# Optimization experiments

Hardware: AMD Instinct MI355X
Metric: run time of the kernel (lower is better)

The kernel has to match this reference:

```python
import jax, jax.numpy as jnp
import numpy as np
from jax import lax

B, S, C, V, D, NC, NF, H = 8, 1024, 512, 512, 512, 512, 2, 8
TAU = 1.0


def conv1d(x, w, b, stride=1, pad=0):
    # x [B,C,S], w [O,I,K]
    y = lax.conv_general_dilated(x, w, (stride,), [(pad, pad)],
                                 dimension_numbers=('NCW', 'OIW', 'NCW'))
    return y + b[None, :, None]


def conv_transpose1d(x, w, b):
    # torch ConvTranspose1d(k=2, s=2); w [I,O,K]
    y = lax.conv_transpose(x, w, (2,), 'VALID',
                           dimension_numbers=('NCW', 'IOW', 'NCW'),
                           transpose_kernel=True)
    return y + b[None, :, None]


def resblock(x, ws, bs):
    h = x
    for i in range(3):
        h = conv1d(jax.nn.elu(h), ws[i], bs[i])
    return h + x


def layernorm(x, g, b):
    m = x.mean(-1, keepdims=True)
    v = ((x - m) ** 2).mean(-1, keepdims=True)
    return (x - m) / jnp.sqrt(v + 1e-5) * g + b


def mha(x, in_w, in_b, out_w, out_b):
    # x [S,B,C], torch nn.MultiheadAttention (eval, no dropout)
    S_, B_, C_ = x.shape
    hd = C_ // H
    qkv = x @ in_w.T + in_b            # [S,B,3C]
    q, k, v = jnp.split(qkv, 3, axis=-1)
    q = q.reshape(S_, B_, H, hd)
    k = k.reshape(S_, B_, H, hd)
    v = v.reshape(S_, B_, H, hd)
    att = jnp.einsum('sbhd,tbhd->bhst', q, k) / np.sqrt(hd).astype(np.float32)
    att = jax.nn.softmax(att, axis=-1)
    o = jnp.einsum('bhst,tbhd->sbhd', att, v).reshape(S_, B_, C_)
    return o @ out_w.T + out_b


def setup_inputs() -> dict:
    key = jax.random.key(0)
    ks = iter(jax.random.split(key, 64))
    def w(shape, s=0.02):
        return jax.random.normal(next(ks), shape, jnp.float32) * s
    inp = {}
    inp['x'] = jax.random.randint(next(ks), (B, S), 0, V, jnp.int32)
    inp['embed'] = w((V, C)).at[0].set(0.0)  # padding_idx=0
    inp['enc_res_w'] = w((3, C, C, 1)); inp['enc_res_b'] = w((3, C))
    inp['enc_in_w'] = w((3 * C, C)); inp['enc_in_b'] = w((3 * C,))
    inp['enc_out_w'] = w((C, C)); inp['enc_out_b'] = w((C,))
    inp['enc_ln_g'] = jnp.ones((C,), jnp.float32); inp['enc_ln_b'] = jnp.zeros((C,), jnp.float32)
    inp['enc_down_w'] = w((NF, C, C, 2)); inp['enc_down_b'] = w((NF, C))
    inp['e2q_w'] = w((D, C, 3)); inp['e2q_b'] = w((D,))
    inp['codebook'] = jax.random.normal(next(ks), (D, NC), jnp.float32)  # [dim, n_embed]
    inp['q2d_w'] = w((C, D, 3)); inp['q2d_b'] = w((C,))
    inp['dec_res_w'] = w((NF, 3, C, C, 1)); inp['dec_res_b'] = w((NF, 3, C))
    inp['dec_in_w'] = w((NF, 3 * C, C)); inp['dec_in_b'] = w((NF, 3 * C))
    inp['dec_out_w'] = w((NF, C, C)); inp['dec_out_b'] = w((NF, C))
    inp['dec_ln_g'] = jnp.ones((NF, C), jnp.float32); inp['dec_ln_b'] = jnp.zeros((NF, C), jnp.float32)
    inp['dec_up_w'] = w((NF, C, C, 2)); inp['dec_up_b'] = w((NF, C))
    return inp


def reference(x, embed, enc_res_w, enc_res_b, enc_in_w, enc_in_b, enc_out_w,
              enc_out_b, enc_ln_g, enc_ln_b, enc_down_w, enc_down_b, e2q_w,
              e2q_b, codebook, q2d_w, q2d_b, dec_res_w, dec_res_b, dec_in_w,
              dec_in_b, dec_out_w, dec_out_b, dec_ln_g, dec_ln_b, dec_up_w,
              dec_up_b):
    # ---- encode ----
    h = embed[x]                       # [B,S,C]
    h = h.transpose(0, 2, 1)           # [B,C,S]
    h = resblock(h, enc_res_w, enc_res_b)
    t = h.transpose(2, 0, 1)           # [S,B,C]
    t = layernorm(mha(t, enc_in_w, enc_in_b, enc_out_w, enc_out_b) + t,
                  enc_ln_g, enc_ln_b)
    h = t.transpose(1, 2, 0)           # [B,C,S]
    for i in range(NF):
        h = conv1d(h, enc_down_w[i], enc_down_b[i], stride=2)
    h = conv1d(h, e2q_w, e2q_b, pad=1)  # [B,D,S4]
    z_e = h.transpose(0, 2, 1)          # [B,S4,D]
    # ---- VQ quantize (eval) ----
    flat = z_e.reshape(-1, D)
    dist = ((flat ** 2).sum(1, keepdims=True)
            - 2.0 * flat @ codebook
            + (codebook ** 2).sum(0)[None, :])
    ids = jnp.argmin(dist, axis=1).reshape(z_e.shape[0], -1)  # [B,S4]
    q = codebook.T[ids]                 # [B,S4,D]
    diff = jnp.mean((lax.stop_gradient(q) - z_e) ** 2)
    z = z_e + lax.stop_gradient(q - z_e)  # straight-through
    # ---- decode ----
    h = z.transpose(0, 2, 1)            # [B,D,S4]
    h = conv1d(h, q2d_w, q2d_b, pad=1)  # [B,C,S4]
    for i in range(NF):
        h = resblock(h, dec_res_w[i], dec_res_b[i])
        t = h.transpose(2, 0, 1)
        t = layernorm(mha(t, dec_in_w[i], dec_in_b[i], dec_out_w[i], dec_out_b[i]) + t,
                      dec_ln_g[i], dec_ln_b[i])
        h = t.transpose(1, 2, 0)
        h = conv_transpose1d(h, dec_up_w[i], dec_up_b[i])
    h = h.transpose(0, 2, 1)            # [B,S,C]
    logp = jax.nn.log_softmax(h / TAU, axis=-1)
    return logp, z, diff, ids
```

## Files before the change

### kernel.cpp

```cpp
#include <hip/hip_runtime.h>
#include <hip/hip_bf16.h>


static constexpr size_t SLOT = 4194304;

typedef short bf16x8 __attribute__((ext_vector_type(8)));
typedef float f32x4  __attribute__((ext_vector_type(4)));

__device__ __forceinline__ float eluf(float x) { return x > 0.f ? x : expm1f(x); }
__device__ __forceinline__ short f2bf(float v) {
  unsigned u = __float_as_uint(v);
  return (short)((u + 0x7FFFu + ((u >> 16) & 1u)) >> 16);
}
__device__ __forceinline__ float bf2f(short s) {
  return __uint_as_float(((unsigned)(unsigned short)s) << 16);
}

__global__ __launch_bounds__(256) void gemm_k(
    const float* __restrict__ A, const float* __restrict__ W,
    const float* __restrict__ bias, const float* __restrict__ res,
    float* __restrict__ Y, int P, int K, int O,
    int act, int accum, int smod, int shift, int ystride, int yoff,
    int WS, int nseg)
{
  __shared__ alignas(16) float As[16][68];
  __shared__ alignas(16) float Bs[16][68];
  const int tid = threadIdx.x;
  const int bp = blockIdx.x * 64, bo = blockIdx.y * 64;
  const int tx = tid & 15, ty = tid >> 4;
  const int srow = tid >> 2, skq = (tid & 3) << 2;
  float vout[4][4];

  for (int seg = 0; seg < nseg; seg++) {
    const int sh = (nseg == 3) ? (seg - 1) : shift;
    const float* Wseg = (nseg == 3) ? (W + (size_t)seg * 262144) : W;
    float acc[4][4];
#pragma unroll
    for (int i = 0; i < 4; i++)
#pragma unroll
      for (int j = 0; j < 4; j++) acc[i][j] = 0.f;

    bool aok = true;
    if (smod) { const int s = (bp + srow) & (smod - 1); aok = ((unsigned)(s + sh) < (unsigned)smod); }
    const float* arow = A + (size_t)(bp + srow + sh) * K;
    const float* brow = Wseg + (size_t)(bo + srow) * WS;

    float4 pa = aok ? *(const float4*)&arow[skq] : make_float4(0.f, 0.f, 0.f, 0.f);
    float4 pb = *(const float4*)&brow[skq];

    for (int k0 = 0; k0 < K; k0 += 16) {
      if (act) { pa.x = eluf(pa.x); pa.y = eluf(pa.y); pa.z = eluf(pa.z); pa.w = eluf(pa.w); }
      __syncthreads();
      As[skq + 0][srow] = pa.x; As[skq + 1][srow] = pa.y;
      As[skq + 2][srow] = pa.z; As[skq + 3][srow] = pa.w;
      Bs[skq + 0][srow] = pb.x; Bs[skq + 1][srow] = pb.y;
      Bs[skq + 2][srow] = pb.z; Bs[skq + 3][srow] = pb.w;
      __syncthreads();
      const int kn = (k0 + 16 < K) ? (k0 + 16 + skq) : (k0 + skq);
      pa = aok ? *(const float4*)&arow[kn] : make_float4(0.f, 0.f, 0.f, 0.f);
      pb = *(const float4*)&brow[kn];
#pragma unroll
      for (int kk2 = 0; kk2 < 16; kk2++) {
        const float4 av = *(const float4*)&As[kk2][ty * 4];
        const float4 bv = *(const float4*)&Bs[kk2][tx * 4];
        const float a_[4] = {av.x, av.y, av.z, av.w};
        const float b_[4] = {bv.x, bv.y, bv.z, bv.w};
#pragma unroll
        for (int i = 0; i < 4; i++)
#pragma unroll
          for (int j = 0; j < 4; j++) acc[i][j] += a_[i] * b_[j];
      }
    }
    if (seg == 0) {
#pragma unroll
      for (int i = 0; i < 4; i++)
#pragma unroll
        for (int j = 0; j < 4; j++) {
          float t = acc[i][j];
          if (nseg == 3 && bias) t += bias[bo + tx * 4 + j];
          vout[i][j] = t;
        }
    } else {
#pragma unroll
      for (int i = 0; i < 4; i++)
#pragma unroll
        for (int j = 0; j < 4; j++) vout[i][j] = acc[i][j] + vout[i][j];
    }
  }
#pragma unroll
  for (int i = 0; i < 4; i++) {
    const int p = bp + ty * 4 + i;
    const size_t yrow = (size_t)p * ystride + yoff;
#pragma unroll
    for (int j = 0; j < 4; j++) {
      const int o = bo + tx * 4 + j;
      float v = vout[i][j];
      if (nseg == 1) {
        if (bias) v += bias[o];
        if (res)  v += res[(size_t)p * O + o];
        if (accum) v += Y[yrow * O + o];
      }
      Y[yrow * O + o] = v;
    }
  }
}

static inline void launch_gemm(hipStream_t st, const float* A, const float* W,
                               const float* bias, const float* res, float* Y,
                               int P, int K, int O, int act, int accum,
                               int smod, int shift, int ystride, int yoff,
                               int WS, int nseg)
{
  dim3 g(P / 64, O / 64);
  gemm_k<<<g, 256, 0, st>>>(A, W, bias, res, Y, P, K, O, act, accum, smod, shift,
                            ystride, yoff, WS, nseg);
}

__global__ __launch_bounds__(256) void bgemm_k(
    const short* __restrict__ A, const short* __restrict__ W,
    const float* __restrict__ bias, const float* __restrict__ res,
    float* __restrict__ Y, int P, int O, int accum,
    int smod, int shift, int ystride, int yoff,
    short* __restrict__ Yb, int bact, int k3)
{
  __shared__ short As[4096];
  __shared__ short Bs[4096];
  const int tid = threadIdx.x;
  const int lane = tid & 63, wid = tid >> 6;
  const int wr = wid >> 1, wc = wid & 1;
  const int bp = blockIdx.x * 64, bo = blockIdx.y * 64;
  f32x4 acc[2][2];
#pragma unroll
  for (int mi = 0; mi < 2; mi++)
#pragma unroll
    for (int ni = 0; ni < 2; ni++) acc[mi][ni] = (f32x4){0.f, 0.f, 0.f, 0.f};

  const int nseg = k3 ? 3 : 1;
  for (int seg = 0; seg < nseg; seg++) {
    const int sh = k3 ? (seg - 1) : shift;
    const int sm = k3 ? 256 : smod;
    const short* Wseg = W + (size_t)seg * 262144;
    for (int k0 = 0; k0 < 512; k0 += 64) {
#pragma unroll
      for (int c0 = 0; c0 < 2; c0++) {
        const int c = tid + c0 * 256;
        const int row = c >> 3, kc = c & 7;
        int soff = (row << 6) + (kc << 3); soff ^= (row & 7) << 3;
        const int p = bp + row;
        bf16x8 av = {0, 0, 0, 0, 0, 0, 0, 0};
        bool ok = true;
        if (sm) { const int s = p & (sm - 1); ok = ((unsigned)(s + sh) < (unsigned)sm); }
        if (ok) av = *(const bf16x8*)&A[(size_t)(p + sh) * 512 + k0 + (kc << 3)];
        *(bf16x8*)&As[soff] = av;
        *(bf16x8*)&Bs[soff] = *(const bf16x8*)&Wseg[(size_t)(bo + row) * 512 + k0 + (kc << 3)];
      }
      __syncthreads();
#pragma unroll
      for (int ks = 0; ks < 2; ks++) {
        bf16x8 af[2], bfr[2];
#pragma unroll
        for (int mi = 0; mi < 2; mi++) {
          const int row = wr * 32 + mi * 16 + (lane & 15);
          int soff = (row << 6) + (ks << 5) + ((lane >> 4) << 3);
          soff ^= (row & 7) << 3;
          af[mi] = *(const bf16x8*)&As[soff];
        }
#pragma unroll
        for (int ni = 0; ni < 2; ni++) {
          const int row = wc * 32 + ni * 16 + (lane & 15);
          int soff = (row << 6) + (ks << 5) + ((lane >> 4) << 3);
          soff ^= (row & 7) << 3;
          bfr[ni] = *(const bf16x8*)&Bs[soff];
        }
#pragma unroll
        for (int mi = 0; mi < 2; mi++)
#pragma unroll
          for (int ni = 0; ni < 2; ni++)
            acc[mi][ni] = __builtin_amdgcn_mfma_f32_16x16x32_bf16(af[mi], bfr[ni], acc[mi][ni], 0, 0, 0);
      }
      __syncthreads();
    }
  }
#pragma unroll
  for (int mi = 0; mi < 2; mi++)
#pragma unroll
    for (int ni = 0; ni < 2; ni++)
#pragma unroll
      for (int r = 0; r < 4; r++) {
        const int p = bp + wr * 32 + mi * 16 + ((lane >> 4) << 2) + r;
        const int o = bo + wc * 32 + ni * 16 + (lane & 15);
        float v = acc[mi][ni][r];
        if (bias) v += bias[o];
        if (res)  v += res[(size_t)p * O + o];
        const size_t yi = ((size_t)p * ystride + yoff) * O + o;
        if (accum) v += Y[yi];
        if (Y) Y[yi] = v;
        if (Yb) Yb[yi] = f2bf(bact ? eluf(v) : v);
      }
}

__global__ __launch_bounds__(512) void battn_k(
    const short* __restrict__ qkv, float* __restrict__ Oa,
    short* __restrict__ Ob, int S)
{
  __shared__ short sq[8192];
  __shared__ short sk[4096];
  __shared__ short svt[4096];
  const int tid = threadIdx.x;
  const int lane = tid & 63, w = tid >> 6;
  const int bl = blockIdx.y >> 3, h = blockIdx.y & 7;
  const int q0 = blockIdx.x * 128;
  const short* base = qkv + (size_t)bl * S * 1536 + h * 64;

  {
    const int row = tid >> 2, c0 = (tid & 3) << 4;
    const short* src = base + (size_t)(q0 + row) * 1536 + c0;
    bf16x8 v0 = *(const bf16x8*)&src[0];
    bf16x8 v1 = *(const bf16x8*)&src[8];
#pragma unroll
    for (int e = 0; e < 8; e++) {
      v0[e] = f2bf(bf2f(v0[e]) * 0.125f);
      v1[e] = f2bf(bf2f(v1[e]) * 0.125f);
    }
    int s0 = (row << 6) + c0;       s0 ^= (row & 7) << 3;
    int s1 = (row << 6) + c0 + 8;   s1 ^= (row & 7) << 3;
    *(bf16x8*)&sq[s0] = v0; *(bf16x8*)&sq[s1] = v1;
  }
  __syncthreads();
  bf16x8 af[2];
#pragma unroll
  for (int ks = 0; ks < 2; ks++) {
    const int row = (w << 4) + (lane & 15);
    int soff = (row << 6) + (((lane >> 4) + 4 * ks) << 3);
    soff ^= (row & 7) << 3;
    af[ks] = *(const bf16x8*)&sq[soff];
  }

  f32x4 oacc[4];
#pragma unroll
  for (int dt = 0; dt < 4; dt++) oacc[dt] = (f32x4){0.f, 0.f, 0.f, 0.f};
  float m[4], l[4];
#pragma unroll
  for (int r = 0; r < 4; r++) { m[r] = -INFINITY; l[r] = 0.f; }

  for (int t0 = 0; t0 < S; t0 += 64) {
    __syncthreads();
    if (tid < 256) {
      const int row = tid >> 2, c0 = (tid & 3) << 4;
      const short* ksrc = base + (size_t)(t0 + row) * 1536 + 512 + c0;
      int s0 = (row << 6) + c0;       s0 ^= (row & 7) << 3;
      int s1 = (row << 6) + c0 + 8;   s1 ^= (row & 7) << 3;
      *(bf16x8*)&sk[s0] = *(const bf16x8*)&ksrc[0];
      *(bf16x8*)&sk[s1] = *(const bf16x8*)&ksrc[8];
    } else {
      const int t = tid - 256;
      const int row = t >> 2, c0 = (t & 3) << 4;
      const short* vsrc = base + (size_t)(t0 + row) * 1536 + 1024 + c0;
      const bf16x8 va0 = *(const bf16x8*)&vsrc[0];
      const bf16x8 va1 = *(const bf16x8*)&vsrc[8];
#pragma unroll
      for (int i = 0; i < 16; i++) {
        const int dd = c0 + i;
        int so = (dd << 6) + row;
        so ^= ((dd & 7) ^ (((dd >> 4) & 3) << 1)) << 3;
        svt[so] = (i < 8) ? va0[i & 7] : va1[i & 7];
      }
    }
    __syncthreads();
    f32x4 sacc[4];
#pragma unroll
    for (int ct = 0; ct < 4; ct++) {
      sacc[ct] = (f32x4){0.f, 0.f, 0.f, 0.f};
#pragma unroll
      for (int ks = 0; ks < 2; ks++) {
        const int row = (ct << 4) + (lane & 15);
        int soff = (row << 6) + (((lane >> 4) + 4 * ks) << 3);
        soff ^= (row & 7) << 3;
        const bf16x8 bk = *(const bf16x8*)&sk[soff];
        sacc[ct] = __builtin_amdgcn_mfma_f32_16x16x32_bf16(af[ks], bk, sacc[ct], 0, 0, 0);
      }
    }
    float p[4][4]; float corr[4];
#pragma unroll
    for (int r = 0; r < 4; r++) {
      float mx = fmaxf(fmaxf(sacc[0][r], sacc[1][r]), fmaxf(sacc[2][r], sacc[3][r]));
      mx = fmaxf(mx, __shfl_xor(mx, 1));
      mx = fmaxf(mx, __shfl_xor(mx, 2));
      mx = fmaxf(mx, __shfl_xor(mx, 4));
      mx = fmaxf(mx, __shfl_xor(mx, 8));
      const float newm = fmaxf(m[r], mx);
      corr[r] = expf(m[r] - newm);
      float psum = 0.f;
#pragma unroll
      for (int ct = 0; ct < 4; ct++) { p[ct][r] = expf(sacc[ct][r] - newm); psum += p[ct][r]; }
      psum += __shfl_xor(psum, 1);
      psum += __shfl_xor(psum, 2);
      psum += __shfl_xor(psum, 4);
      psum += __shfl_xor(psum, 8);
      l[r] = l[r] * corr[r] + psum;
      m[r] = newm;
#pragma unroll
      for (int dt = 0; dt < 4; dt++) oacc[dt][r] *= corr[r];
    }
#pragma unroll
    for (int r = 0; r < 4; r++)
#pragma unroll
      for (int ct = 0; ct < 4; ct++) {
        const int q = (w << 4) + ((lane >> 4) << 2) + r;
        const int kv = (ct << 4) + (lane & 15);
        int so = (q << 6) + kv; so ^= (q & 7) << 3;
        sq[so] = f2bf(p[ct][r]);
      }
#pragma unroll
    for (int ks = 0; ks < 2; ks++) {
      const int prow = (w << 4) + (lane & 15);
      int poff = (prow << 6) + (((lane >> 4) + 4 * ks) << 3);
      poff ^= (prow & 7) << 3;
      const bf16x8 pa = *(const bf16x8*)&sq[poff];
#pragma unroll
      for (int dt = 0; dt < 4; dt++) {
        const int vrow = (dt << 4) + (lane & 15);
        int voff = (vrow << 6) + (((lane >> 4) + 4 * ks) << 3);
        voff ^= ((vrow & 7) ^ (((vrow >> 4) & 3) << 1)) << 3;
        const bf16x8 bv = *(const bf16x8*)&svt[voff];
        oacc[dt] = __builtin_amdgcn_mfma_f32_16x16x32_bf16(pa, bv, oacc[dt], 0, 0, 0);
      }
    }
  }
#pragma unroll
  for (int r = 0; r < 4; r++) {
    const float inv = 1.f / l[r];
    const int q = (w << 4) + ((lane >> 4) << 2) + r;
    const size_t rowbase = (size_t)(bl * S + q0 + q) * 512 + h * 64;
#pragma unroll
    for (int dt = 0; dt < 4; dt++) {
      const int d = (dt << 4) + (lane & 15);
      const float ov = oacc[dt][r] * inv;
      if (Oa) Oa[rowbase + d] = ov;
      if (Ob) Ob[rowbase + d] = f2bf(ov);
    }
  }
}

__global__ __launch_bounds__(256) void cast_k(const float* __restrict__ src,
    short* __restrict__ dst, int act)
{
  const size_t i = ((size_t)blockIdx.x * 256 + threadIdx.x) * 8;
  float4 a = *(const float4*)&src[i];
  float4 b = *(const float4*)&src[i + 4];
  if (act) {
    a.x = eluf(a.x); a.y = eluf(a.y); a.z = eluf(a.z); a.w = eluf(a.w);
    b.x = eluf(b.x); b.y = eluf(b.y); b.z = eluf(b.z); b.w = eluf(b.w);
  }
  bf16x8 o;
  o[0] = f2bf(a.x); o[1] = f2bf(a.y); o[2] = f2bf(a.z); o[3] = f2bf(a.w);
  o[4] = f2bf(b.x); o[5] = f2bf(b.y); o[6] = f2bf(b.z); o[7] = f2bf(b.w);
  *(bf16x8*)&dst[i] = o;
}

__global__ __launch_bounds__(256) void q2dw_k(const float* __restrict__ src, short* __restrict__ dst)
{
  const int idx = blockIdx.x * 256 + threadIdx.x;
  const int w = idx >> 18, rem = idx & 262143;
  const int o = rem >> 9, k = rem & 511;
  dst[idx] = f2bf(src[(size_t)o * 1536 + k * 3 + w]);
}

__global__ __launch_bounds__(256) void upw_k(const float* __restrict__ src, short* __restrict__ dst)
{
  const int idx = blockIdx.x * 256 + threadIdx.x;
  const int mi = idx >> 18, f = mi >> 1, kq = mi & 1;
  const int rem = idx & 262143;
  const int o = rem >> 9, i2 = rem & 511;
  dst[idx] = f2bf(src[(size_t)f * 524288 + (size_t)i2 * 1024 + o * 2 + kq]);
}

__global__ __launch_bounds__(256) void downw_k(const float* __restrict__ src, float* __restrict__ dst)
{
  const int idx = blockIdx.x * 256 + threadIdx.x;
  const int i = idx & 511, ks = (idx >> 9) & 1, o = idx >> 10;
  dst[idx] = src[(size_t)o * 1024 + i * 2 + ks];
}

__global__ __launch_bounds__(256) void e2qw_k(const float* __restrict__ src, float* __restrict__ dst)
{
  const int idx = blockIdx.x * 256 + threadIdx.x;
  const int w = idx >> 18, rem = idx & 262143;
  const int o = rem >> 9, k = rem & 511;
  dst[idx] = src[(size_t)o * 1536 + k * 3 + w];
}

__global__ __launch_bounds__(256) void cbt_k(const float* __restrict__ src, float* __restrict__ dst)
{
  const int idx = blockIdx.x * 256 + threadIdx.x;
  const int n = idx >> 9, d = idx & 511;
  dst[idx] = src[(size_t)d * 512 + n];
}

__global__ __launch_bounds__(256) void ln_k(const float* __restrict__ X,
    const float* __restrict__ g, const float* __restrict__ bta,
    float* __restrict__ Y, short* __restrict__ Ob)
{
  const int row = blockIdx.x * 4 + (threadIdx.x >> 6);
  const int lane = threadIdx.x & 63;
  const float* x = X + (size_t)row * 512;
  float v[8]; float s = 0.f;
#pragma unroll
  for (int i = 0; i < 8; i++) { v[i] = x[lane + i * 64]; s += v[i]; }
#pragma unroll
  for (int off = 1; off < 64; off <<= 1) s += __shfl_xor(s, off);
  const float mean = s * (1.f / 512.f);
  float vs = 0.f;
#pragma unroll
  for (int i = 0; i < 8; i++) { const float d = v[i] - mean; vs += d * d; }
#pragma unroll
  for (int off = 1; off < 64; off <<= 1) vs += __shfl_xor(vs, off);
  const float rstd = 1.f / sqrtf(vs * (1.f / 512.f) + 1e-5f);
  float* y = Y ? (Y + (size_t)row * 512) : nullptr;
#pragma unroll
  for (int i = 0; i < 8; i++) {
    const int c = lane + i * 64;
    const float o = (v[i] - mean) * rstd * g[c] + bta[c];
    if (y) y[c] = o;
    if (Ob) Ob[(size_t)row * 512 + c] = f2bf(o);
  }
}

__global__ __launch_bounds__(256) void lsm_k(const float* __restrict__ X,
    float* __restrict__ out)
{
  const int row = blockIdx.x * 4 + (threadIdx.x >> 6);
  const int lane = threadIdx.x & 63;
  const float* x = X + (size_t)row * 512;
  float v[8]; float mx = -3.0e38f;
#pragma unroll
  for (int i = 0; i < 8; i++) { v[i] = x[lane + i * 64]; mx = fmaxf(mx, v[i]); }
#pragma unroll
  for (int off = 1; off < 64; off <<= 1) mx = fmaxf(mx, __shfl_xor(mx, off));
  float sum = 0.f;
#pragma unroll
  for (int i = 0; i < 8; i++) sum += expf(v[i] - mx);
#pragma unroll
  for (int off = 1; off < 64; off <<= 1) sum += __shfl_xor(sum, off);
  const float ls = logf(sum);
  float* y = out + (size_t)row * 512;
#pragma unroll
  for (int i = 0; i < 8; i++) y[lane + i * 64] = v[i] - mx - ls;
}

__global__ __launch_bounds__(256) void embed_k(const int* __restrict__ x,
    const float* __restrict__ emb, float* __restrict__ out, short* __restrict__ outb)
{
  const int i = blockIdx.x * 256 + threadIdx.x;
  const int p = i >> 7, c4 = i & 127;
  const int id = x[p];
  const float4 v = *(const float4*)&emb[(size_t)id * 512 + c4 * 4];
  *(float4*)&out[(size_t)p * 512 + c4 * 4] = v;
  short* ob = outb + (size_t)p * 512 + c4 * 4;
  ob[0] = f2bf(eluf(v.x)); ob[1] = f2bf(eluf(v.y));
  ob[2] = f2bf(eluf(v.z)); ob[3] = f2bf(eluf(v.w));
}

__global__ __launch_bounds__(64) void cnorm_k(const float* __restrict__ cbT, float* __restrict__ cn)
{
  const int n = blockIdx.x; const int lane = threadIdx.x;
  float s = 0.f;
#pragma unroll
  for (int i = 0; i < 8; i++) {
    const float v = cbT[(size_t)n * 512 + lane + i * 64];
    s += v * v;
  }
#pragma unroll
  for (int off = 1; off < 64; off <<= 1) s += __shfl_xor(s, off);
  if (lane == 0) cn[n] = s;
}

__global__ __launch_bounds__(256) void argmin_k(const float* __restrict__ scores,
    const float* __restrict__ cn, int* __restrict__ ids,
    float* __restrict__ out_ids)
{
  const int row = blockIdx.x * 4 + (threadIdx.x >> 6);
  const int lane = threadIdx.x & 63;
  const float* sr = scores + (size_t)row * 512;
  float best = 3.0e38f; int bi = 0x7fffffff;
#pragma unroll
  for (int i = 0; i < 8; i++) {
    const int n = lane + i * 64;
    const float v = cn[n] - 2.f * sr[n];
    if (v < best || (v == best && n < bi)) { best = v; bi = n; }
  }
#pragma unroll
  for (int off = 1; off < 64; off <<= 1) {
    const float ov = __shfl_xor(best, off);
    const int oi = __shfl_xor(bi, off);
    if (ov < best || (ov == best && oi < bi)) { best = ov; bi = oi; }
  }
  if (lane == 0) { ids[row] = bi; out_ids[row] = (float)bi; }
}

__global__ __launch_bounds__(128) void zq_k(const float* __restrict__ z_e,
    const float* __restrict__ cbT, const int* __restrict__ ids,
    float* __restrict__ zout, short* __restrict__ zb, float* __restrict__ dpart)
{
  __shared__ float red[2];
  const int p = blockIdx.x, t = threadIdx.x;
  const int id = ids[p];
  const float4 ze = *(const float4*)&z_e[(size_t)p * 512 + t * 4];
  const float4 q4 = *(const float4*)&cbT[(size_t)id * 512 + t * 4];
  const float4 dv = make_float4(q4.x - ze.x, q4.y - ze.y, q4.z - ze.z, q4.w - ze.w);
  const float4 z  = make_float4(ze.x + dv.x, ze.y + dv.y, ze.z + dv.z, ze.w + dv.w);
  *(float4*)&zout[(size_t)p * 512 + t * 4] = z;
  short* zo = zb + (size_t)p * 512 + t * 4;
  zo[0] = f2bf(z.x); zo[1] = f2bf(z.y); zo[2] = f2bf(z.z); zo[3] = f2bf(z.w);
  float loc = dv.x * dv.x + dv.y * dv.y + dv.z * dv.z + dv.w * dv.w;
#pragma unroll
  for (int off = 1; off < 64; off <<= 1) loc += __shfl_xor(loc, off);
  const int lane = t & 63, w = t >> 6;
  if (lane == 0) red[w] = loc;
  __syncthreads();
  if (t == 0) dpart[p] = red[0] + red[1];
}

__global__ __launch_bounds__(256) void diffred_k(const float* __restrict__ dpart,
    float* __restrict__ out_diff)
{
  __shared__ float red[4];
  const int t = threadIdx.x;
  float s = 0.f;
#pragma unroll
  for (int i = 0; i < 8; i++) s += dpart[t + i * 256];
#pragma unroll
  for (int off = 1; off < 64; off <<= 1) s += __shfl_xor(s, off);
  if ((t & 63) == 0) red[t >> 6] = s;
  __syncthreads();
  if (t == 0) out_diff[0] = (red[0] + red[1] + red[2] + red[3]) * (1.f / 1048576.f);
}

extern "C" void kernel_launch(void* const* d_in, const int* in_sizes, int n_in,
                              void* d_out, int out_size, void* d_ws, size_t ws_size,
                              hipStream_t stream)
{
  const int*   x         = (const int*)d_in[0];
  const float* embed     = (const float*)d_in[1];
  const float* enc_res_w = (const float*)d_in[2];
  const float* enc_res_b = (const float*)d_in[3];
  const float* enc_in_w  = (const float*)d_in[4];
  const float* enc_in_b  = (const float*)d_in[5];
  const float* enc_out_w = (const float*)d_in[6];
  const float* enc_out_b = (const float*)d_in[7];
  const float* enc_ln_g  = (const float*)d_in[8];
  const float* enc_ln_b  = (const float*)d_in[9];
  const float* enc_down_w= (const float*)d_in[10];
  const float* enc_down_b= (const float*)d_in[11];
  const float* e2q_w     = (const float*)d_in[12];
  const float* e2q_b     = (const float*)d_in[13];
  const float* codebook  = (const float*)d_in[14];
  const float* q2d_w     = (const float*)d_in[15];
  const float* q2d_b     = (const float*)d_in[16];
  const float* dec_res_w = (const float*)d_in[17];
  const float* dec_res_b = (const float*)d_in[18];
  const float* dec_in_w  = (const float*)d_in[19];
  const float* dec_in_b  = (const float*)d_in[20];
  const float* dec_out_w = (const float*)d_in[21];
  const float* dec_out_b = (const float*)d_in[22];
  const float* dec_ln_g  = (const float*)d_in[23];
  const float* dec_ln_b  = (const float*)d_in[24];
  const float* dec_up_w  = (const float*)d_in[25];
  const float* dec_up_b  = (const float*)d_in[26];

  float* ws = (float*)d_ws;
  float* S0   = ws;
  float* S1   = ws + SLOT;
  float* S2   = ws + 2 * SLOT;
  float* QKVb = ws + 3 * SLOT;
  float* cnorm = QKVb + (size_t)8192 * 1536;
  int*   idsI  = (int*)(cnorm + 512);
  float* dpart = (float*)(idsI + 2048);

  float* out      = (float*)d_out;
  float* out_logp = out;
  float* out_z    = out + 4194304;
  float* out_diff = out + 5242880;
  float* out_ids  = out + 5242881;

  short* q2dWb   = (short*)out_logp;
  short* resWb   = q2dWb + 786432;
  short* inWb    = resWb + 1572864;
  short* outWb   = inWb + 1572864;
  short* upWb    = outWb + 524288;
  short* AbA     = upWb + 1048576;
  short* encResWb= AbA + 2097152;
  short* AbB   = (short*)(QKVb + 8388608);
  short* encInWb  = (short*)out_z;
  short* encOutWb = encInWb + 786432;
  float* dsW      = out_z + 524288;
  short* QKVsh = (short*)QKVb;
  float* e2qT  = QKVb;
  float* ds2W  = QKVb + 786432;
  float* cbT   = QKVb + 1310720;
  short* E0    = (short*)QKVb;
  short* E1    = E0 + 4194304;
  short* S2sh  = (short*)S2;

  q2dw_k<<<3072, 256, 0, stream>>>(q2d_w, q2dWb);
  cast_k<<<768, 256, 0, stream>>>(dec_res_w, resWb, 0);
  cast_k<<<768, 256, 0, stream>>>(dec_in_w,  inWb, 0);
  cast_k<<<256, 256, 0, stream>>>(dec_out_w, outWb, 0);
  upw_k<<<4096, 256, 0, stream>>>(dec_up_w, upWb);
  cast_k<<<384, 256, 0, stream>>>(enc_res_w, encResWb, 0);
  cast_k<<<384, 256, 0, stream>>>(enc_in_w,  encInWb, 0);
  cast_k<<<128, 256, 0, stream>>>(enc_out_w, encOutWb, 0);
  downw_k<<<2048, 256, 0, stream>>>(enc_down_w, dsW);

  embed_k<<<4096, 256, 0, stream>>>(x, embed, S0, E0);
  { dim3 g(128, 8);
    bgemm_k<<<g, 256, 0, stream>>>(E0, encResWb,          enc_res_b,        nullptr, nullptr, 8192, 512, 0, 0, 0, 1, 0, E1, 1, 0);
    bgemm_k<<<g, 256, 0, stream>>>(E1, encResWb + 262144, enc_res_b + 512,  nullptr, nullptr, 8192, 512, 0, 0, 0, 1, 0, E0, 1, 0);
    bgemm_k<<<g, 256, 0, stream>>>(E0, encResWb + 524288, enc_res_b + 1024, S0,      S1, 8192, 512, 0, 0, 0, 1, 0, S2sh, 0, 0);
  }
  { dim3 g(128, 24);
    bgemm_k<<<g, 256, 0, stream>>>(S2sh, encInWb, enc_in_b, nullptr, nullptr, 8192, 1536, 0, 0, 0, 1, 0, QKVsh, 0, 0);
  }
  battn_k<<<dim3(8, 64), 512, 0, stream>>>(QKVsh, nullptr, S2sh, 1024);
  { dim3 g(128, 8);
    bgemm_k<<<g, 256, 0, stream>>>(S2sh, encOutWb, enc_out_b, S1, S0, 8192, 512, 0, 0, 0, 1, 0, nullptr, 0, 0);
  }
  e2qw_k<<<3072, 256, 0, stream>>>(e2q_w, e2qT);
  downw_k<<<2048, 256, 0, stream>>>(enc_down_w + 524288, ds2W);
  cbt_k<<<1024, 256, 0, stream>>>(codebook, cbT);
  cnorm_k<<<512, 64, 0, stream>>>(cbT, cnorm);
  ln_k<<<2048, 256, 0, stream>>>(S0, enc_ln_g, enc_ln_b, S1, nullptr);
  launch_gemm(stream, S1, dsW, enc_down_b, nullptr, S2, 4096, 1024, 512, 0, 0, 0, 0, 1, 0, 1024, 1);
  launch_gemm(stream, S2, ds2W, enc_down_b + 512, nullptr, S0, 2048, 1024, 512, 0, 0, 0, 0, 1, 0, 1024, 1);
  launch_gemm(stream, S0, e2qT, e2q_b, nullptr, S2, 2048, 512, 512, 0, 0, 256, 0, 1, 0, 512, 3);
  launch_gemm(stream, S2, cbT, nullptr, nullptr, S1, 2048, 512, 512, 0, 0, 0, 0, 1, 0, 512, 1);
  argmin_k<<<512, 256, 0, stream>>>(S1, cnorm, idsI, out_ids);
  zq_k<<<2048, 128, 0, stream>>>(S2, cbT, idsI, out_z, AbA, dpart);
  diffred_k<<<1, 256, 0, stream>>>(dpart, out_diff);

  { dim3 g(32, 8);
    bgemm_k<<<g, 256, 0, stream>>>(AbA, q2dWb, q2d_b, nullptr, S1, 2048, 512, 0, 256, 0, 1, 0, AbB, 1, 1);
  }
  { dim3 g(32, 8); dim3 gq(32, 24);
    bgemm_k<<<g, 256, 0, stream>>>(AbB, resWb,            dec_res_b,        nullptr, S2, 2048, 512, 0, 0, 0, 1, 0, AbA, 1, 0);
    bgemm_k<<<g, 256, 0, stream>>>(AbA, resWb + 262144,   dec_res_b + 512,  nullptr, S0, 2048, 512, 0, 0, 0, 1, 0, AbB, 1, 0);
    bgemm_k<<<g, 256, 0, stream>>>(AbB, resWb + 524288,   dec_res_b + 1024, S1,      S2, 2048, 512, 0, 0, 0, 1, 0, AbA, 0, 0);
    bgemm_k<<<gq, 256, 0, stream>>>(AbA, inWb,            dec_in_b,         nullptr, nullptr, 2048, 1536, 0, 0, 0, 1, 0, QKVsh, 0, 0);
    battn_k<<<dim3(2, 64), 512, 0, stream>>>(QKVsh, nullptr, AbB, 256);
    bgemm_k<<<g, 256, 0, stream>>>(AbB, outWb,            dec_out_b,        S2, S1, 2048, 512, 0, 0, 0, 1, 0, nullptr, 0, 0);
    ln_k<<<512, 256, 0, stream>>>(S1, dec_ln_g, dec_ln_b, S2, AbA);
    bgemm_k<<<g, 256, 0, stream>>>(AbA, upWb,             dec_up_b, nullptr, S0, 2048, 512, 0, 0, 0, 2, 0, AbB, 1, 0);
    bgemm_k<<<g, 256, 0, stream>>>(AbA, upWb + 262144,    dec_up_b, nullptr, S0, 2048, 512, 0, 0, 0, 2, 1, AbB, 1, 0);
  }
  { dim3 g(64, 8); dim3 gq(64, 24);
    bgemm_k<<<g, 256, 0, stream>>>(AbB, resWb + 786432,   dec_res_b + 1536, nullptr, S1, 4096, 512, 0, 0, 0, 1, 0, AbA, 1, 0);
    bgemm_k<<<g, 256, 0, stream>>>(AbA, resWb + 1048576,  dec_res_b + 2048, nullptr, S2, 4096, 512, 0, 0, 0, 1, 0, AbB, 1, 0);
    bgemm_k<<<g, 256, 0, stream>>>(AbB, resWb + 1310720,  dec_res_b + 2560, S0,      S1, 4096, 512, 0, 0, 0, 1, 0, AbA, 0, 0);
    bgemm_k<<<gq, 256, 0, stream>>>(AbA, inWb + 786432,   dec_in_b + 1536,  nullptr, nullptr, 4096, 1536, 0, 0, 0, 1, 0, QKVsh, 0, 0);
    battn_k<<<dim3(4, 64), 512, 0, stream>>>(QKVsh, nullptr, AbB, 512);
    bgemm_k<<<g, 256, 0, stream>>>(AbB, outWb + 262144,   dec_out_b + 512,  S1, S0, 4096, 512, 0, 0, 0, 1, 0, nullptr, 0, 0);
    ln_k<<<1024, 256, 0, stream>>>(S0, dec_ln_g + 512, dec_ln_b + 512, S1, AbA);
    bgemm_k<<<g, 256, 0, stream>>>(AbA, upWb + 524288,    dec_up_b + 512, nullptr, S0, 4096, 512, 0, 0, 0, 2, 0, nullptr, 0, 0);
    bgemm_k<<<g, 256, 0, stream>>>(AbA, upWb + 786432,    dec_up_b + 512, nullptr, S0, 4096, 512, 0, 0, 0, 2, 1, nullptr, 0, 0);
  }
  lsm_k<<<2048, 256, 0, stream>>>(S0, out_logp);
}
```

Baseline: 792.9 us.

## Double-buffer shared memory and register-prefetch tiles in both GEMM kernels

```diff
diff --git a/kernel.cpp b/kernel.cpp
--- a/kernel.cpp
+++ b/kernel.cpp
@@ -23,68 +23,83 @@
     int act, int accum, int smod, int shift, int ystride, int yoff,
     int WS, int nseg)
 {
-  __shared__ alignas(16) float As[16][68];
-  __shared__ alignas(16) float Bs[16][68];
+  __shared__ alignas(16) float As[2][16][68];
+  __shared__ alignas(16) float Bs[2][16][68];
   const int tid = threadIdx.x;
   const int bp = blockIdx.x * 64, bo = blockIdx.y * 64;
   const int tx = tid & 15, ty = tid >> 4;
   const int srow = tid >> 2, skq = (tid & 3) << 2;
-  float vout[4][4];
-
-  for (int seg = 0; seg < nseg; seg++) {
-    const int sh = (nseg == 3) ? (seg - 1) : shift;
-    const float* Wseg = (nseg == 3) ? (W + (size_t)seg * 262144) : W;
-    float acc[4][4];
-#pragma unroll
-    for (int i = 0; i < 4; i++)
-#pragma unroll
-      for (int j = 0; j < 4; j++) acc[i][j] = 0.f;
-
-    bool aok = true;
-    if (smod) { const int s = (bp + srow) & (smod - 1); aok = ((unsigned)(s + sh) < (unsigned)smod); }
-    const float* arow = A + (size_t)(bp + srow + sh) * K;
-    const float* brow = Wseg + (size_t)(bo + srow) * WS;
-
-    float4 pa = aok ? *(const float4*)&arow[skq] : make_float4(0.f, 0.f, 0.f, 0.f);
-    float4 pb = *(const float4*)&brow[skq];
-
-    for (int k0 = 0; k0 < K; k0 += 16) {
-      if (act) { pa.x = eluf(pa.x); pa.y = eluf(pa.y); pa.z = eluf(pa.z); pa.w = eluf(pa.w); }
-      __syncthreads();
-      As[skq + 0][srow] = pa.x; As[skq + 1][srow] = pa.y;
-      As[skq + 2][srow] = pa.z; As[skq + 3][srow] = pa.w;
-      Bs[skq + 0][srow] = pb.x; Bs[skq + 1][srow] = pb.y;
-      Bs[skq + 2][srow] = pb.z; Bs[skq + 3][srow] = pb.w;
-      __syncthreads();
-      const int kn = (k0 + 16 < K) ? (k0 + 16 + skq) : (k0 + skq);
-      pa = aok ? *(const float4*)&arow[kn] : make_float4(0.f, 0.f, 0.f, 0.f);
-      pb = *(const float4*)&brow[kn];
-#pragma unroll
-      for (int kk2 = 0; kk2 < 16; kk2++) {
-        const float4 av = *(const float4*)&As[kk2][ty * 4];
-        const float4 bv = *(const float4*)&Bs[kk2][tx * 4];
-        const float a_[4] = {av.x, av.y, av.z, av.w};
-        const float b_[4] = {bv.x, bv.y, bv.z, bv.w};
+  float vout[4][4], acc[4][4];
+#pragma unroll
+  for (int i = 0; i < 4; i++)
+#pragma unroll
+    for (int j = 0; j < 4; j++) acc[i][j] = 0.f;
+
+  const float* arow = nullptr; const float* brow = nullptr; bool aok = true;
+  auto seg_setup = [&](int s) {
+    const int sh = (nseg == 3) ? (s - 1) : shift;
+    const float* Wseg = (nseg == 3) ? (W + (size_t)s * 262144) : W;
+    aok = true;
+    if (smod) { const int ss = (bp + srow) & (smod - 1); aok = ((unsigned)(ss + sh) < (unsigned)smod); }
+    arow = A + (size_t)(bp + srow + sh) * K;
+    brow = Wseg + (size_t)(bo + srow) * WS;
+  };
+  seg_setup(0);
+  float4 pa = aok ? *(const float4*)&arow[skq] : make_float4(0.f, 0.f, 0.f, 0.f);
+  float4 pb = *(const float4*)&brow[skq];
+
+  const int ips = K >> 4;
+  const int niter = nseg * ips;
+  int lkk = 0, lseg = 0, cur = 0, ckk = 0, cseg = 0;
+
+  for (int it = 0; it < niter; ++it) {
+    if (act) { pa.x = eluf(pa.x); pa.y = eluf(pa.y); pa.z = eluf(pa.z); pa.w = eluf(pa.w); }
+    As[cur][skq + 0][srow] = pa.x; As[cur][skq + 1][srow] = pa.y;
+    As[cur][skq + 2][srow] = pa.z; As[cur][skq + 3][srow] = pa.w;
+    Bs[cur][skq + 0][srow] = pb.x; Bs[cur][skq + 1][srow] = pb.y;
+    Bs[cur][skq + 2][srow] = pb.z; Bs[cur][skq + 3][srow] = pb.w;
+    __syncthreads();
+    if (it + 1 < niter) {
+      lkk += 16;
+      if (lkk == K) { lkk = 0; seg_setup(++lseg); }
+      pa = aok ? *(const float4*)&arow[lkk + skq] : make_float4(0.f, 0.f, 0.f, 0.f);
+      pb = *(const float4*)&brow[lkk + skq];
+    }
+#pragma unroll
+    for (int kk2 = 0; kk2 < 16; kk2++) {
+      const float4 av = *(const float4*)&As[cur][kk2][ty * 4];
+      const float4 bv = *(const float4*)&Bs[cur][kk2][tx * 4];
+      const float a_[4] = {av.x, av.y, av.z, av.w};
+      const float b_[4] = {bv.x, bv.y, bv.z, bv.w};
+#pragma unroll
+      for (int i = 0; i < 4; i++)
+#pragma unroll
+        for (int j = 0; j < 4; j++) acc[i][j] += a_[i] * b_[j];
+    }
+    cur ^= 1;
+    ckk += 16;
+    if (ckk == K) {
+      ckk = 0;
+      if (cseg == 0) {
 #pragma unroll
         for (int i = 0; i < 4; i++)
 #pragma unroll
-          for (int j = 0; j < 4; j++) acc[i][j] += a_[i] * b_[j];
-      }
-    }
-    if (seg == 0) {
+          for (int j = 0; j < 4; j++) {
+            float t = acc[i][j];
+            if (nseg == 3 && bias) t += bias[bo + tx * 4 + j];
+            vout[i][j] = t;
+          }
+      } else {
+#pragma unroll
+        for (int i = 0; i < 4; i++)
+#pragma unroll
+          for (int j = 0; j < 4; j++) vout[i][j] = acc[i][j] + vout[i][j];
+      }
 #pragma unroll
       for (int i = 0; i < 4; i++)
 #pragma unroll
-        for (int j = 0; j < 4; j++) {
-          float t = acc[i][j];
-          if (nseg == 3 && bias) t += bias[bo + tx * 4 + j];
-          vout[i][j] = t;
-        }
-    } else {
-#pragma unroll
-      for (int i = 0; i < 4; i++)
-#pragma unroll
-        for (int j = 0; j < 4; j++) vout[i][j] = acc[i][j] + vout[i][j];
+        for (int j = 0; j < 4; j++) acc[i][j] = 0.f;
+      cseg++;
     }
   }
 #pragma unroll
@@ -123,8 +138,8 @@
     int smod, int shift, int ystride, int yoff,
     short* __restrict__ Yb, int bact, int k3)
 {
-  __shared__ short As[4096];
-  __shared__ short Bs[4096];
+  __shared__ short As[2][4096];
+  __shared__ short Bs[2][4096];
   const int tid = threadIdx.x;
   const int lane = tid & 63, wid = tid >> 6;
   const int wr = wid >> 1, wc = wid & 1;
@@ -136,50 +151,68 @@
     for (int ni = 0; ni < 2; ni++) acc[mi][ni] = (f32x4){0.f, 0.f, 0.f, 0.f};
 
   const int nseg = k3 ? 3 : 1;
-  for (int seg = 0; seg < nseg; seg++) {
+  const int niter = nseg * 8;
+  bf16x8 rA[2], rB[2];
+
+  auto stage_load = [&](int it) {
+    const int seg = it >> 3, k0 = (it & 7) << 6;
     const int sh = k3 ? (seg - 1) : shift;
     const int sm = k3 ? 256 : smod;
     const short* Wseg = W + (size_t)seg * 262144;
-    for (int k0 = 0; k0 < 512; k0 += 64) {
-#pragma unroll
-      for (int c0 = 0; c0 < 2; c0++) {
-        const int c = tid + c0 * 256;
-        const int row = c >> 3, kc = c & 7;
-        int soff = (row << 6) + (kc << 3); soff ^= (row & 7) << 3;
-        const int p = bp + row;
-        bf16x8 av = {0, 0, 0, 0, 0, 0, 0, 0};
-        bool ok = true;
-        if (sm) { const int s = p & (sm - 1); ok = ((unsigned)(s + sh) < (unsigned)sm); }
-        if (ok) av = *(const bf16x8*)&A[(size_t)(p + sh) * 512 + k0 + (kc << 3)];
-        *(bf16x8*)&As[soff] = av;
-        *(bf16x8*)&Bs[soff] = *(const bf16x8*)&Wseg[(size_t)(bo + row) * 512 + k0 + (kc << 3)];
-      }
-      __syncthreads();
-#pragma unroll
-      for (int ks = 0; ks < 2; ks++) {
-        bf16x8 af[2], bfr[2];
-#pragma unroll
-        for (int mi = 0; mi < 2; mi++) {
-          const int row = wr * 32 + mi * 16 + (lane & 15);
-          int soff = (row << 6) + (ks << 5) + ((lane >> 4) << 3);
-          soff ^= (row & 7) << 3;
-          af[mi] = *(const bf16x8*)&As[soff];
-        }
-#pragma unroll
-        for (int ni = 0; ni < 2; ni++) {
-          const int row = wc * 32 + ni * 16 + (lane & 15);
-          int soff = (row << 6) + (ks << 5) + ((lane >> 4) << 3);
-          soff ^= (row & 7) << 3;
-          bfr[ni] = *(const bf16x8*)&Bs[soff];
-        }
-#pragma unroll
-        for (int mi = 0; mi < 2; mi++)
-#pragma unroll
-          for (int ni = 0; ni < 2; ni++)
-            acc[mi][ni] = __builtin_amdgcn_mfma_f32_16x16x32_bf16(af[mi], bfr[ni], acc[mi][ni], 0, 0, 0);
-      }
-      __syncthreads();
-    }
+#pragma unroll
+    for (int c0 = 0; c0 < 2; c0++) {
+      const int c = tid + c0 * 256;
+      const int row = c >> 3, kc = c & 7;
+      const int p = bp + row;
+      bf16x8 av = {0, 0, 0, 0, 0, 0, 0, 0};
+      bool ok = true;
+      if (sm) { const int s = p & (sm - 1); ok = ((unsigned)(s + sh) < (unsigned)sm); }
+      if (ok) av = *(const bf16x8*)&A[(size_t)(p + sh) * 512 + k0 + (kc << 3)];
+      rA[c0] = av;
+      rB[c0] = *(const bf16x8*)&Wseg[(size_t)(bo + row) * 512 + k0 + (kc << 3)];
+    }
+  };
+  auto stage_write = [&](int cb) {
+#pragma unroll
+    for (int c0 = 0; c0 < 2; c0++) {
+      const int c = tid + c0 * 256;
+      const int row = c >> 3, kc = c & 7;
+      int soff = (row << 6) + (kc << 3); soff ^= (row & 7) << 3;
+      *(bf16x8*)&As[cb][soff] = rA[c0];
+      *(bf16x8*)&Bs[cb][soff] = rB[c0];
+    }
+  };
+
+  stage_load(0);
+  int cur = 0;
+  for (int it = 0; it < niter; ++it) {
+    stage_write(cur);
+    __syncthreads();
+    if (it + 1 < niter) stage_load(it + 1);
+#pragma unroll
+    for (int ks = 0; ks < 2; ks++) {
+      bf16x8 af[2], bfr[2];
+#pragma unroll
+      for (int mi = 0; mi < 2; mi++) {
+        const int row = wr * 32 + mi * 16 + (lane & 15);
+        int soff = (row << 6) + (ks << 5) + ((lane >> 4) << 3);
+        soff ^= (row & 7) << 3;
+        af[mi] = *(const bf16x8*)&As[cur][soff];
+      }
+#pragma unroll
+      for (int ni = 0; ni < 2; ni++) {
+        const int row = wc * 32 + ni * 16 + (lane & 15);
+        int soff = (row << 6) + (ks << 5) + ((lane >> 4) << 3);
+        soff ^= (row & 7) << 3;
+        bfr[ni] = *(const bf16x8*)&Bs[cur][soff];
+      }
+#pragma unroll
+      for (int mi = 0; mi < 2; mi++)
+#pragma unroll
+        for (int ni = 0; ni < 2; ni++)
+          acc[mi][ni] = __builtin_amdgcn_mfma_f32_16x16x32_bf16(af[mi], bfr[ni], acc[mi][ni], 0, 0, 0);
+    }
+    cur ^= 1;
   }
 #pragma unroll
   for (int mi = 0; mi < 2; mi++)
```

Result: faster. 729.4 us (-8.0%).
